# Performance work log

Hardware: AMD Instinct MI355X
Metric: run time of the kernel (lower is better)

## Reference

```python
import jax, jax.numpy as jnp
import numpy as np

MODES = (16, 16)
EMBED_DIM = 64
NUM_HEADS = 8


def spectral_conv(x, w):
    """FNO-style spectral conv. x: [B,S,Ci,H,W]; w: [Ci,Co,mx,my,2] (real/imag)."""
    wc = w[..., 0] + 1j * w[..., 1]
    H, W = x.shape[-2], x.shape[-1]
    mx, my = wc.shape[2], wc.shape[3]
    xf = jnp.fft.rfft2(x)                                   # [B,S,Ci,H,W//2+1]
    of = jnp.einsum('bsixy,ioxy->bsoxy', xf[..., :mx, :my], wc)
    out_f = jnp.zeros(x.shape[:2] + (wc.shape[1], H, W // 2 + 1), dtype=of.dtype)
    out_f = out_f.at[..., :mx, :my].set(of)
    return jnp.fft.irfft2(out_f, s=(H, W))


def log_cpb_bias(n_sub_x, n_sub_y, w1, b1, w2):
    """Swin-v2-style log-spaced continuous position bias -> [heads, S, S]."""
    cx = jnp.arange(n_sub_x, dtype=jnp.float32)
    cy = jnp.arange(n_sub_y, dtype=jnp.float32)
    coords = jnp.stack(jnp.meshgrid(cx, cy, indexing='ij'), axis=-1).reshape(-1, 2)
    rel = coords[:, None, :] - coords[None, :, :]           # [S,S,2]
    rel = jnp.sign(rel) * jnp.log1p(jnp.abs(rel))
    h = jax.nn.relu(rel @ w1 + b1)                          # [S,S,hidden]
    bias = h @ w2                                           # [S,S,heads]
    return jnp.transpose(bias, (2, 0, 1))


def _unflatten(f, num_heads, embed_dim):
    # [B,S,h*d,H,W] -> [B,h,S,d,H,W]
    B, S = f.shape[0], f.shape[1]
    f = f.reshape(B, S, num_heads, embed_dim, f.shape[-2], f.shape[-1])
    return jnp.transpose(f, (0, 2, 1, 3, 4, 5))


def setup_inputs() -> dict:
    key = jax.random.key(0)
    ks = jax.random.split(key, 9)
    B, S, D, H, W = 2, 64, EMBED_DIM, 32, 32
    hd = NUM_HEADS * D
    mx, my = MODES
    scale = 0.02
    return {
        'seq': jax.random.normal(ks[0], (B, S, D, H, W), dtype=jnp.float32),
        'wq': scale * jax.random.normal(ks[1], (D, hd, mx, my, 2), dtype=jnp.float32),
        'wk': scale * jax.random.normal(ks[2], (D, hd, mx, my, 2), dtype=jnp.float32),
        'wv': scale * jax.random.normal(ks[3], (D, hd, mx, my, 2), dtype=jnp.float32),
        'wo': scale * jax.random.normal(ks[4], (hd, D, mx, my, 2), dtype=jnp.float32),
        'cpb_w1': scale * jax.random.normal(ks[5], (2, D), dtype=jnp.float32),
        'cpb_b1': jnp.zeros((D,), dtype=jnp.float32),
        'cpb_w2': scale * jax.random.normal(ks[6], (D, NUM_HEADS), dtype=jnp.float32),
        'n_sub_x': 8,
        'n_sub_y': 8,
    }


def reference(seq, wq, wk, wv, wo, cpb_w1, cpb_b1, cpb_w2, n_sub_x, n_sub_y):
    q = _unflatten(spectral_conv(seq, wq), NUM_HEADS, EMBED_DIM)  # [B,h,S,d,H,W]
    k = _unflatten(spectral_conv(seq, wk), NUM_HEADS, EMBED_DIM)
    v = _unflatten(spectral_conv(seq, wv), NUM_HEADS, EMBED_DIM)

    bias = log_cpb_bias(n_sub_x, n_sub_y, cpb_w1, cpb_b1, cpb_w2)  # [h,S,S]

    d, H, W = q.shape[-3], q.shape[-2], q.shape[-1]
    scale = 1.0 / jnp.sqrt(jnp.asarray(d * H * W, dtype=q.dtype))
    scores = jnp.einsum('bhqdxy,bhkdxy->bhqk', q, k) * scale + bias[None]
    attn = jax.nn.softmax(scores, axis=-1)
    sa = jnp.einsum('bhqk,bhkdxy->bhqdxy', attn, v)          # [B,h,S,d,H,W]

    # _flatten: [B,h,S,d,H,W] -> [B,S,h*d,H,W]
    sa = jnp.transpose(sa, (0, 2, 1, 3, 4, 5))
    B, S = sa.shape[0], sa.shape[1]
    sa = sa.reshape(B, S, NUM_HEADS * EMBED_DIM, H, W)
    return spectral_conv(sa, wo)
```

## Files before the change

kernel.cpp:

```cpp
#include <hip/hip_runtime.h>

#define TWO_PI 6.28318530717958647692f

#define NH 8
#define CH 128
#define NCH 2

#define OFF_XM   0ull
#define OFF_WTA  (OFF_XM + 8388608ull)
#define OFF_WTB  (OFF_WTA + 16777216ull)
#define OFF_PO   (OFF_WTB + 16777216ull)
#define OFF_ATTN (OFF_PO + 16777216ull)
#define WS_TOTAL (OFF_ATTN + 262144ull)

typedef short bf16x8 __attribute__((ext_vector_type(8)));
typedef float f32x4 __attribute__((ext_vector_type(4)));
#define MFMA_B16(a, b, c) __builtin_amdgcn_mfma_f32_16x16x32_bf16(a, b, c, 0, 0, 0)

__device__ __forceinline__ float bl(unsigned u) { return __uint_as_float(u << 16); }
__device__ __forceinline__ unsigned short f2b(float f) {
    unsigned u = __float_as_uint(f);
    return (unsigned short)((u + 0x7fffu + ((u >> 16) & 1u)) >> 16);
}
__device__ __forceinline__ unsigned pack2(float lo, float hi) {
    return (unsigned)f2b(lo) | ((unsigned)f2b(hi) << 16);
}

__device__ __forceinline__ bf16x8 mkfrag(const unsigned* __restrict__ Wt, int co_l, int ri,
                                         int ci0, bool dc) {
    unsigned a0 = Wt[(ci0 + 0) * 64 + (co_l ^ (ci0 + 0))];
    unsigned a1 = Wt[(ci0 + 1) * 64 + (co_l ^ (ci0 + 1))];
    unsigned a2 = Wt[(ci0 + 2) * 64 + (co_l ^ (ci0 + 2))];
    unsigned a3 = Wt[(ci0 + 3) * 64 + (co_l ^ (ci0 + 3))];
    uint4 r;
    if (ri) {
        if (dc) { r.x = 0u; r.y = 0u; r.z = 0u; r.w = 0u; }
        else {
            r.x = (a0 >> 16) | (a0 << 16); r.y = (a1 >> 16) | (a1 << 16);
            r.z = (a2 >> 16) | (a2 << 16); r.w = (a3 >> 16) | (a3 << 16);
        }
    } else {
        r.x = a0 ^ 0x80000000u; r.y = a1 ^ 0x80000000u;
        r.z = a2 ^ 0x80000000u; r.w = a3 ^ 0x80000000u;
    }
    return __builtin_bit_cast(bf16x8, r);
}

__global__ __launch_bounds__(256) void k_transpose2(const float* __restrict__ srcA, unsigned* __restrict__ dstA, int kindA,
                                                    const float* __restrict__ srcB, unsigned* __restrict__ dstB, int kindB,
                                                    int m0) {
    const float* in = (blockIdx.z == 0) ? srcA : srcB;
    unsigned* outp = (blockIdx.z == 0) ? dstA : dstB;
    int kind = (blockIdx.z == 0) ? kindA : kindB;
    __shared__ unsigned T[16][65];
    int tid = threadIdx.x;
    int r0 = blockIdx.x * 64;
    int ci, h;
    if (kind == 2) { h = r0 >> 12; ci = (r0 >> 6) & 63; }
    else           { ci = r0 >> 9; h = (r0 >> 6) & 7; }
    int ml0 = blockIdx.y * 16;
    int u = (m0 + ml0) >> 4;
    const float4* in4 = (const float4*)in;
    float fac1 = (kind == 0) ? 1.41421356f : 1.f;
    float facu = (kind == 0) ? (u > 0 ? 0.70710678f : 1.f)
               : (kind == 1) ? (u > 0 ? 0.5f : 1.f) : 1.f;
    #pragma unroll
    for (int p = 0; p < 2; ++p) {
        int f = tid + p * 256;
        int row = f >> 3, mc2 = (f & 7) * 2;
        float4 v = in4[(size_t)(r0 + row) * 128 + ((m0 + ml0) >> 1) + (f & 7)];
        float fac0 = (mc2 > 0) ? fac1 : facu;
        T[mc2][row] = pack2(v.x * fac0, v.y * fac0);
        T[mc2 + 1][row] = pack2(v.z * fac1, v.w * fac1);
    }
    __syncthreads();
    #pragma unroll
    for (int p = 0; p < 4; ++p) {
        int f = tid + p * 256;
        int ml = f >> 6, co = f & 63;
        outp[((size_t)((ml0 + ml) * 8 + h) << 12) + ci * 64 + co] = T[ml][co];
    }
}

__global__ __launch_bounds__(256) void k_rfft_y(const float* __restrict__ seq,
                                                float2* __restrict__ T) {
    __shared__ float c32[32], s32[32];
    __shared__ float fld[32][33];
    int tid = threadIdx.x;
    int bc = blockIdx.x;
    if (tid < 32) { float s, c; __sincosf(TWO_PI * tid / 32.0f, &s, &c); c32[tid] = c; s32[tid] = s; }
    float4 v = ((const float4*)(seq + (size_t)bc * 1024))[tid];
    int x = tid >> 3, y4 = (tid & 7) * 4;
    fld[x][y4] = v.x; fld[x][y4 + 1] = v.y; fld[x][y4 + 2] = v.z; fld[x][y4 + 3] = v.w;
    __syncthreads();
    float2* op = T + (size_t)bc * 512;
    #pragma unroll
    for (int p = 0; p < 2; ++p) {
        int e = tid + p * 256;
        int xx = e >> 4, vv = e & 15;
        float sr = 0.f, si = 0.f;
        #pragma unroll
        for (int y = 0; y < 32; ++y) {
            float f = fld[xx][y];
            int ph = (vv * y) & 31;
            sr = fmaf(f, c32[ph], sr);
            si = fmaf(-f, s32[ph], si);
        }
        float2 t; t.x = sr; t.y = si;
        op[e] = t;
    }
}

__global__ __launch_bounds__(256) void k_rfft_x(const float2* __restrict__ T,
                                                unsigned short* __restrict__ XM) {
    __shared__ float c32[32], s32[32];
    __shared__ float2 t[8][512];
    int tid = threadIdx.x;
    int cig = blockIdx.x;
    int bs = blockIdx.y;
    if (tid < 32) { float s, c; __sincosf(TWO_PI * tid / 32.0f, &s, &c); c32[tid] = c; s32[tid] = s; }
    const float4* src = (const float4*)(T + ((size_t)bs * 64 + cig * 8) * 512);
    #pragma unroll
    for (int p = 0; p < 8; ++p) {
        int idx = tid + p * 256;
        float4 w = src[idx];
        int ch = idx >> 8, r2 = idx & 255;
        float2 t0; t0.x = w.x; t0.y = w.y;
        float2 t1; t1.x = w.z; t1.y = w.w;
        t[ch][r2 * 2] = t0; t[ch][r2 * 2 + 1] = t1;
    }
    __syncthreads();
    int u = tid >> 4, vv = tid & 15;
    unsigned outw[8];
    for (int ch = 0; ch < 8; ++ch) {
        float xr = 0.f, xi = 0.f;
        #pragma unroll
        for (int x = 0; x < 32; ++x) {
            float2 tv = t[ch][x * 16 + vv];
            int ph = (u * x) & 31;
            float c = c32[ph], s = s32[ph];
            xr += tv.x * c + tv.y * s;
            xi += tv.y * c - tv.x * s;
        }
        outw[ch] = pack2(xr, xi);
    }
    uint4* op = (uint4*)(XM + (((size_t)tid * 128 + bs) * 64 + cig * 8) * 2);
    uint4 a, b;
    a.x = outw[0]; a.y = outw[1]; a.z = outw[2]; a.w = outw[3];
    b.x = outw[4]; b.y = outw[5]; b.z = outw[6]; b.w = outw[7];
    op[0] = a; op[1] = b;
}

__global__ __launch_bounds__(512) void k_qks(const unsigned short* __restrict__ XM,
                                             const unsigned* __restrict__ WQ,
                                             const unsigned* __restrict__ WK,
                                             float* __restrict__ part, int mbase) {
    __shared__ __align__(16) unsigned char Xs[16384];
    __shared__ __align__(16) unsigned Wq[4096];
    __shared__ __align__(16) unsigned Wk[4096];
    unsigned char* Qs = Xs;
    unsigned char* Ks = (unsigned char*)Wq;
    int tid = threadIdx.x;
    int mg = blockIdx.x, h = blockIdx.y, b = blockIdx.z;
    int lane = tid & 63, w = tid >> 6;
    int lr = lane & 15, lg = lane >> 4;
    int wr = w & 1, wc = w >> 1;
    int sxa = (lr & 7) << 4;
    int ri = lr & 1;
    f32x4 zf = {0.f, 0.f, 0.f, 0.f};
    f32x4 sacc[2];
    sacc[0] = zf; sacc[1] = zf;
    for (int mm = 0; mm < 4; ++mm) {
        int ml = mg * 4 + mm;
        int mode = mbase + ml;
        bool dc = (mode == 0);
        __syncthreads();
        {
            const unsigned short* xg = XM + ((size_t)mode * 128 + b * 64) * 128;
            #pragma unroll
            for (int p = 0; p < 2; ++p) {
                int g = tid + p * 512; int row = g >> 4, c16 = g & 15;
                uint4 v = *(const uint4*)(xg + row * 128 + c16 * 8);
                *(uint4*)(Xs + row * 256 + ((c16 * 16) ^ ((row & 7) << 4))) = v;
            }
        }
        {
            const unsigned* tq = WQ + ((size_t)(ml * 8 + h) << 12);
            const unsigned* tk = WK + ((size_t)(ml * 8 + h) << 12);
            #pragma unroll
            for (int p = 0; p < 16; ++p) {
                int idx = tid + p * 512;
                int r = idx & 4095;
                int ci = r >> 6, co = r & 63;
                if (idx < 4096) Wq[ci * 64 + (co ^ ci)] = tq[r];
                else            Wk[ci * 64 + (co ^ ci)] = tk[r];
            }
        }
        __syncthreads();
        f32x4 qa[2][2], ka[2][2];
        {
            #pragma unroll
            for (int m = 0; m < 2; ++m)
                #pragma unroll
                for (int n = 0; n < 2; ++n) { qa[m][n] = zf; ka[m][n] = zf; }
            #pragma unroll
            for (int ks = 0; ks < 4; ++ks) {
                int kb = (ks * 64 + lg * 16) ^ sxa;
                int ci0 = ks * 16 + lg * 4;
                bf16x8 a0 = *(const bf16x8*)(Xs + (wr * 32 + lr) * 256 + kb);
                bf16x8 a1 = *(const bf16x8*)(Xs + (wr * 32 + 16 + lr) * 256 + kb);
                #pragma unroll
                for (int n = 0; n < 2; ++n) {
                    int co_l = wc * 16 + n * 8 + (lr >> 1);
                    bf16x8 bq = mkfrag(Wq, co_l, ri, ci0, dc);
                    bf16x8 bk = mkfrag(Wk, co_l, ri, ci0, dc);
                    qa[0][n] = MFMA_B16(a0, bq, qa[0][n]);
                    qa[1][n] = MFMA_B16(a1, bq, qa[1][n]);
                    ka[0][n] = MFMA_B16(a0, bk, ka[0][n]);
                    ka[1][n] = MFMA_B16(a1, bk, ka[1][n]);
                }
            }
        }
        __syncthreads();
        {
            #pragma unroll
            for (int m = 0; m < 2; ++m)
                #pragma unroll
                for (int n = 0; n < 2; ++n) {
                    int colb = (wc * 32 + n * 16 + lr) * 2;
                    #pragma unroll
                    for (int r = 0; r < 4; ++r) {
                        int row = wr * 32 + m * 16 + lg * 4 + r;
                        int swz = (row & 7) << 4;
                        *(unsigned short*)(Qs + row * 256 + (colb ^ swz)) = f2b(qa[m][n][r]);
                        *(unsigned short*)(Ks + row * 256 + (colb ^ swz)) = f2b(ka[m][n][r]);
                    }
                }
        }
        __syncthreads();
        {
            #pragma unroll
            for (int ks = 0; ks < 4; ++ks) {
                int kb = (ks * 64 + lg * 16) ^ sxa;
                bf16x8 a0 = *(const bf16x8*)(Qs + (wr * 32 + lr) * 256 + kb);
                bf16x8 a1 = *(const bf16x8*)(Qs + (wr * 32 + 16 + lr) * 256 + kb);
                bf16x8 b0 = *(const bf16x8*)(Ks + (wc * 16 + lr) * 256 + kb);
                sacc[0] = MFMA_B16(a0, b0, sacc[0]);
                sacc[1] = MFMA_B16(a1, b0, sacc[1]);
            }
        }
    }
    float* pp = part + (((size_t)((mbase >> 2) + mg) * 16 + b * 8 + h) << 12);
    #pragma unroll
    for (int m = 0; m < 2; ++m)
        #pragma unroll
        for (int r = 0; r < 4; ++r)
            pp[(wr * 32 + m * 16 + lg * 4 + r) * 64 + wc * 16 + lr] = sacc[m][r];
}

__global__ void k_softmax(const float* __restrict__ part,
                          const float* __restrict__ w1, const float* __restrict__ b1,
                          const float* __restrict__ w2, unsigned short* __restrict__ attnb) {
    int j = threadIdx.x;
    int i = blockIdx.x;
    int bh = blockIdx.y;
    int h = bh & 7;
    float s = 0.f;
    for (int mg = 0; mg < 64; ++mg)
        s += part[(((size_t)mg * 16 + bh) * 64 + i) * 64 + j];
    float dx = (float)((i >> 3) - (j >> 3));
    float dy = (float)((i & 7) - (j & 7));
    float rx = (dx > 0.f ? 1.f : (dx < 0.f ? -1.f : 0.f)) * log1pf(fabsf(dx));
    float ry = (dy > 0.f ? 1.f : (dy < 0.f ? -1.f : 0.f)) * log1pf(fabsf(dy));
    float bias = 0.f;
    for (int l = 0; l < 64; ++l) {
        float hv = fmaxf(rx * w1[l] + ry * w1[64 + l] + b1[l], 0.f);
        bias = fmaf(hv, w2[l * NH + h], bias);
    }
    s = s * (1.0f / 262144.0f) + bias;
    float m = s;
    for (int o = 32; o >= 1; o >>= 1) m = fmaxf(m, __shfl_xor(m, o));
    float e = expf(s - m);
    float t = e;
    for (int o = 32; o >= 1; o >>= 1) t += __shfl_xor(t, o);
    attnb[((size_t)bh * 64 + i) * 64 + j] = f2b(e / t);
}

__global__ __launch_bounds__(512) void k_savo(const unsigned short* __restrict__ XM,
                                              const unsigned* __restrict__ WV,
                                              const unsigned* __restrict__ WO,
                                              const unsigned short* __restrict__ attnb,
                                              float* __restrict__ outf, int mbase) {
    __shared__ __align__(16) unsigned char Xs[16384];
    __shared__ __align__(16) unsigned Wv[4096];
    __shared__ __align__(16) unsigned Wo[4096];
    unsigned char* Vt = (unsigned char*)Wv;
    unsigned char* Ss = (unsigned char*)Wv;
    int tid = threadIdx.x;
    int ml = blockIdx.x, b = blockIdx.y;
    int mode = mbase + ml;
    bool dc = (mode == 0);
    int lane = tid & 63, w = tid >> 6;
    int lr = lane & 15, lg = lane >> 4;
    int wr = w & 1, wc = w >> 1;
    int sxa = (lr & 7) << 4;
    int ri = lr & 1;
    f32x4 zf = {0.f, 0.f, 0.f, 0.f};
    {
        const unsigned short* xg = XM + ((size_t)mode * 128 + b * 64) * 128;
        #pragma unroll
        for (int p = 0; p < 2; ++p) {
            int g = tid + p * 512; int row = g >> 4, c16 = g & 15;
            uint4 v = *(const uint4*)(xg + row * 128 + c16 * 8);
            *(uint4*)(Xs + row * 256 + ((c16 * 16) ^ ((row & 7) << 4))) = v;
        }
    }
    f32x4 oacc[2][2];
    oacc[0][0] = zf; oacc[0][1] = zf; oacc[1][0] = zf; oacc[1][1] = zf;
    for (int h = 0; h < NH; ++h) {
        __syncthreads();
        {
            const unsigned* tv = WV + ((size_t)(ml * 8 + h) << 12);
            const unsigned* to = WO + ((size_t)(ml * 8 + h) << 12);
            #pragma unroll
            for (int p = 0; p < 16; ++p) {
                int idx = tid + p * 512;
                int r = idx & 4095;
                int ci = r >> 6, co = r & 63;
                if (idx < 4096) Wv[ci * 64 + (co ^ ci)] = tv[r];
                else            Wo[ci * 64 + (co ^ ci)] = to[r];
            }
        }
        bf16x8 af[2][2];
        #pragma unroll
        for (int m = 0; m < 2; ++m)
            #pragma unroll
            for (int ks = 0; ks < 2; ++ks) {
                int irow = wr * 32 + m * 16 + lr;
                af[m][ks] = *(const bf16x8*)(attnb + (((size_t)(b * 8 + h) * 64 + irow) * 64 + ks * 32 + lg * 8));
            }
        __syncthreads();
        f32x4 va[2][2];
        {
            va[0][0] = zf; va[0][1] = zf; va[1][0] = zf; va[1][1] = zf;
            #pragma unroll
            for (int ks = 0; ks < 4; ++ks) {
                int kb = (ks * 64 + lg * 16) ^ sxa;
                int ci0 = ks * 16 + lg * 4;
                bf16x8 a0 = *(const bf16x8*)(Xs + (wr * 32 + lr) * 256 + kb);
                bf16x8 a1 = *(const bf16x8*)(Xs + (wr * 32 + 16 + lr) * 256 + kb);
                #pragma unroll
                for (int n = 0; n < 2; ++n) {
                    int co_l = wc * 16 + n * 8 + (lr >> 1);
                    bf16x8 bb = mkfrag(Wv, co_l, ri, ci0, dc);
                    va[0][n] = MFMA_B16(a0, bb, va[0][n]);
                    va[1][n] = MFMA_B16(a1, bb, va[1][n]);
                }
            }
        }
        __syncthreads();
        {
            #pragma unroll
            for (int m = 0; m < 2; ++m)
                #pragma unroll
                for (int n = 0; n < 2; ++n) {
                    int cp = wc * 32 + n * 16 + lr;
                    int j0 = wr * 32 + m * 16 + lg * 4;
                    uint2 t;
                    t.x = pack2(va[m][n][0], va[m][n][1]);
                    t.y = pack2(va[m][n][2], va[m][n][3]);
                    *(uint2*)(Vt + cp * 128 + ((j0 * 2) ^ ((cp & 7) << 4))) = t;
                }
        }
        __syncthreads();
        f32x4 sa_[2][2];
        {
            sa_[0][0] = zf; sa_[0][1] = zf; sa_[1][0] = zf; sa_[1][1] = zf;
            #pragma unroll
            for (int ks = 0; ks < 2; ++ks) {
                #pragma unroll
                for (int n = 0; n < 2; ++n) {
                    int cp = wc * 32 + n * 16 + lr;
                    bf16x8 bb = *(const bf16x8*)(Vt + cp * 128 + ((ks * 64 + lg * 16) ^ ((cp & 7) << 4)));
                    sa_[0][n] = MFMA_B16(af[0][ks], bb, sa_[0][n]);
                    sa_[1][n] = MFMA_B16(af[1][ks], bb, sa_[1][n]);
                }
            }
        }
        __syncthreads();
        {
            #pragma unroll
            for (int m = 0; m < 2; ++m)
                #pragma unroll
                for (int n = 0; n < 2; ++n) {
                    int colb = (wc * 32 + n * 16 + lr) * 2;
                    #pragma unroll
                    for (int r = 0; r < 4; ++r) {
                        int row = wr * 32 + m * 16 + lg * 4 + r;
                        *(unsigned short*)(Ss + row * 256 + (colb ^ ((row & 7) << 4))) = f2b(sa_[m][n][r]);
                    }
                }
        }
        __syncthreads();
        {
            #pragma unroll
            for (int ks = 0; ks < 4; ++ks) {
                int kb = (ks * 64 + lg * 16) ^ sxa;
                int ci0 = ks * 16 + lg * 4;
                bf16x8 a0 = *(const bf16x8*)(Ss + (wr * 32 + lr) * 256 + kb);
                bf16x8 a1 = *(const bf16x8*)(Ss + (wr * 32 + 16 + lr) * 256 + kb);
                #pragma unroll
                for (int n = 0; n < 2; ++n) {
                    int co_l = wc * 16 + n * 8 + (lr >> 1);
                    bf16x8 bb = mkfrag(Wo, co_l, ri, ci0, false);
                    oacc[0][n] = MFMA_B16(a0, bb, oacc[0][n]);
                    oacc[1][n] = MFMA_B16(a1, bb, oacc[1][n]);
                }
            }
        }
    }
    #pragma unroll
    for (int m = 0; m < 2; ++m)
        #pragma unroll
        for (int n = 0; n < 2; ++n)
            #pragma unroll
            for (int r = 0; r < 4; ++r) {
                int i = wr * 32 + m * 16 + lg * 4 + r;
                int c2p = wc * 32 + n * 16 + lr;
                outf[((size_t)mode * 128 + b * 64 + i) * 128 + c2p] = oacc[m][n][r];
            }
}

__global__ __launch_bounds__(256) void k_irfft_v(const float* __restrict__ outf,
                                                 float2* __restrict__ G) {
    __shared__ float c32[32], s32[32];
    __shared__ float2 mf[256][8];
    int tid = threadIdx.x;
    int cg = blockIdx.x;
    int bs = blockIdx.y;
    if (tid < 32) { float s, c; __sincosf(TWO_PI * tid / 32.0f, &s, &c); c32[tid] = c; s32[tid] = s; }
    #pragma unroll
    for (int p = 0; p < 4; ++p) {
        int idx = tid + p * 256;
        int mode = idx >> 2, q = idx & 3;
        float4 v = *(const float4*)(outf + ((size_t)mode * 128 + bs) * 128 + cg * 16 + q * 4);
        float2 t0; t0.x = v.x; t0.y = v.y;
        float2 t1; t1.x = v.z; t1.y = v.w;
        mf[mode][q * 2] = t0; mf[mode][q * 2 + 1] = t1;
    }
    __syncthreads();
    #pragma unroll 1
    for (int p = 0; p < 2; ++p) {
        int e = tid + p * 256;
        int u = e >> 5, y = e & 31;
        #pragma unroll 1
        for (int ch = 0; ch < 8; ++ch) {
            float2 f0 = mf[u * 16][ch];
            float fr0 = f0.x;
            float fi0 = (u == 0) ? 0.f : f0.y;
            float ssr = 0.5f * fr0, ssi = 0.5f * fi0;
            #pragma unroll
            for (int v = 1; v < 16; ++v) {
                float2 f = mf[u * 16 + v][ch];
                int ph = (v * y) & 31;
                float c = c32[ph], s = s32[ph];
                ssr += f.x * c - f.y * s;
                ssi += f.x * s + f.y * c;
            }
            float2 g; g.x = ssr; g.y = ssi;
            G[(((size_t)u * 128 + bs) * 64 + cg * 8 + ch) * 32 + y] = g;
        }
    }
}

__global__ __launch_bounds__(256) void k_irfft_u(const float2* __restrict__ G,
                                                 float* __restrict__ out) {
    __shared__ float c32[32], s32[32];
    __shared__ float2 Gs[16][8][32];
    int tid = threadIdx.x;
    int cg = blockIdx.x;
    int bs = blockIdx.y;
    if (tid < 32) { float s, c; __sincosf(TWO_PI * tid / 32.0f, &s, &c); c32[tid] = c; s32[tid] = s; }
    #pragma unroll
    for (int p = 0; p < 8; ++p) {
        int idx = tid + p * 256;
        int y2 = idx & 15, ch = (idx >> 4) & 7, u = idx >> 7;
        float4 v = *(const float4*)((const float*)G + ((((size_t)u * 128 + bs) * 64 + cg * 8 + ch) * 32 + y2 * 2) * 2);
        float2 t0; t0.x = v.x; t0.y = v.y;
        float2 t1; t1.x = v.z; t1.y = v.w;
        Gs[u][ch][y2 * 2] = t0; Gs[u][ch][y2 * 2 + 1] = t1;
    }
    __syncthreads();
    #pragma unroll 1
    for (int p = 0; p < 4; ++p) {
        int pos = tid + p * 256;
        int x = pos >> 5, y = pos & 31;
        #pragma unroll 1
        for (int ch = 0; ch < 8; ++ch) {
            float acc = 0.f;
            #pragma unroll
            for (int u = 0; u < 16; ++u) {
                float2 g = Gs[u][ch][y];
                int ph = (u * x) & 31;
                acc += g.x * c32[ph] - g.y * s32[ph];
            }
            out[((size_t)(bs * 64 + cg * 8 + ch)) * 1024 + x * 32 + y] = acc * (1.0f / 512.0f);
        }
    }
}

extern "C" void kernel_launch(void* const* d_in, const int* in_sizes, int n_in,
                              void* d_out, int out_size, void* d_ws, size_t ws_size,
                              hipStream_t stream) {
    (void)in_sizes; (void)n_in; (void)out_size;
    const float* seq = (const float*)d_in[0];
    const float* wq = (const float*)d_in[1];
    const float* wk = (const float*)d_in[2];
    const float* wv = (const float*)d_in[3];
    const float* wo = (const float*)d_in[4];
    const float* cw1 = (const float*)d_in[5];
    const float* cb1 = (const float*)d_in[6];
    const float* cw2 = (const float*)d_in[7];
    float* out = (float*)d_out;
    char* ws = (char*)d_ws;
    if (ws_size < WS_TOTAL) return;

    unsigned short* XM = (unsigned short*)(ws + OFF_XM);
    unsigned* WTA = (unsigned*)(ws + OFF_WTA);
    unsigned* WTB = (unsigned*)(ws + OFF_WTB);
    float2* Tbuf = (float2*)(ws + OFF_WTA);
    float2* G = (float2*)(ws + OFF_WTA);
    float* PART = (float*)(ws + OFF_PO);
    float* OUTF = (float*)(ws + OFF_PO);
    unsigned short* ATTNB = (unsigned short*)(ws + OFF_ATTN);

    k_rfft_y<<<dim3(8192), dim3(256), 0, stream>>>(seq, Tbuf);
    k_rfft_x<<<dim3(8, 128), dim3(256), 0, stream>>>(Tbuf, XM);

    for (int c = 0; c < NCH; ++c) {
        int m0 = c * CH;
        k_transpose2<<<dim3(512, CH / 16, 2), dim3(256), 0, stream>>>(wq, WTA, 0, wk, WTB, 0, m0);
        k_qks<<<dim3(CH / 4, NH, 2), dim3(512), 0, stream>>>(XM, WTA, WTB, PART, m0);
    }
    k_softmax<<<dim3(64, 16), dim3(64), 0, stream>>>(PART, cw1, cb1, cw2, ATTNB);

    for (int c = 0; c < NCH; ++c) {
        int m0 = c * CH;
        k_transpose2<<<dim3(512, CH / 16, 2), dim3(256), 0, stream>>>(wv, WTA, 1, wo, WTB, 2, m0);
        k_savo<<<dim3(CH, 2), dim3(512), 0, stream>>>(XM, WTA, WTB, ATTNB, OUTF, m0);
    }
    k_irfft_v<<<dim3(8, 128), dim3(256), 0, stream>>>(OUTF, G);
    k_irfft_u<<<dim3(8, 128), dim3(256), 0, stream>>>(G, out);
}
```

Before: 335.8 us.

## Pre-swizzle spectral layouts in global memory and stage tiles via direct global-to-LDS loads

The producer kernels now write the weight tables and the mode-major spectral activations in the XOR-swizzled order that the shared-memory tiles expect. The consumer kernels can then copy tiles with 16-byte direct global-to-LDS loads instead of a register round trip with per-element swizzled stores. This removes VGPR staging and scalar 4-byte weight stores in the hot loops of the QK and output kernels. It depends on the global_load_lds intrinsic with 16-byte width and on the pre-swizzled layouts matching the read-side indexing exactly.

```diff
diff --git a/kernel.cpp b/kernel.cpp
--- a/kernel.cpp
+++ b/kernel.cpp
@@ -16,6 +16,10 @@
 typedef short bf16x8 __attribute__((ext_vector_type(8)));
 typedef float f32x4 __attribute__((ext_vector_type(4)));
 #define MFMA_B16(a, b, c) __builtin_amdgcn_mfma_f32_16x16x32_bf16(a, b, c, 0, 0, 0)
+
+#define G2L(g, l) __builtin_amdgcn_global_load_lds( \
+    (const __attribute__((address_space(1))) void*)(g), \
+    (__attribute__((address_space(3))) void*)(l), 16, 0, 0)
 
 __device__ __forceinline__ float bl(unsigned u) { return __uint_as_float(u << 16); }
 __device__ __forceinline__ unsigned short f2b(float f) {
@@ -78,7 +82,7 @@
     for (int p = 0; p < 4; ++p) {
         int f = tid + p * 256;
         int ml = f >> 6, co = f & 63;
-        outp[((size_t)((ml0 + ml) * 8 + h) << 12) + ci * 64 + co] = T[ml][co];
+        outp[((size_t)((ml0 + ml) * 8 + h) << 12) + ci * 64 + (co ^ ci)] = T[ml][co];
     }
 }
 
@@ -144,11 +148,13 @@
         }
         outw[ch] = pack2(xr, xi);
     }
-    uint4* op = (uint4*)(XM + (((size_t)tid * 128 + bs) * 64 + cig * 8) * 2);
+    unsigned short* rowp = XM + ((size_t)tid * 128 + bs) * 128;
     uint4 a, b;
     a.x = outw[0]; a.y = outw[1]; a.z = outw[2]; a.w = outw[3];
     b.x = outw[4]; b.y = outw[5]; b.z = outw[6]; b.w = outw[7];
-    op[0] = a; op[1] = b;
+    int sw = bs & 7;
+    *(uint4*)(rowp + ((cig * 2) ^ sw) * 8) = a;
+    *(uint4*)(rowp + ((cig * 2 + 1) ^ sw) * 8) = b;
 }
 
 __global__ __launch_bounds__(512) void k_qks(const unsigned short* __restrict__ XM,
@@ -176,24 +182,15 @@
         bool dc = (mode == 0);
         __syncthreads();
         {
-            const unsigned short* xg = XM + ((size_t)mode * 128 + b * 64) * 128;
+            const char* xg = (const char*)(XM + ((size_t)mode * 128 + b * 64) * 128);
+            const char* tq = (const char*)(WQ + ((size_t)(ml * 8 + h) << 12));
+            const char* tk = (const char*)(WK + ((size_t)(ml * 8 + h) << 12));
             #pragma unroll
             for (int p = 0; p < 2; ++p) {
-                int g = tid + p * 512; int row = g >> 4, c16 = g & 15;
-                uint4 v = *(const uint4*)(xg + row * 128 + c16 * 8);
-                *(uint4*)(Xs + row * 256 + ((c16 * 16) ^ ((row & 7) << 4))) = v;
-            }
-        }
-        {
-            const unsigned* tq = WQ + ((size_t)(ml * 8 + h) << 12);
-            const unsigned* tk = WK + ((size_t)(ml * 8 + h) << 12);
-            #pragma unroll
-            for (int p = 0; p < 16; ++p) {
-                int idx = tid + p * 512;
-                int r = idx & 4095;
-                int ci = r >> 6, co = r & 63;
-                if (idx < 4096) Wq[ci * 64 + (co ^ ci)] = tq[r];
-                else            Wk[ci * 64 + (co ^ ci)] = tk[r];
+                int off = (tid + p * 512) * 16;
+                G2L(xg + off, Xs + off);
+                G2L(tq + off, (char*)Wq + off);
+                G2L(tk + off, (char*)Wk + off);
             }
         }
         __syncthreads();
@@ -307,12 +304,11 @@
     int ri = lr & 1;
     f32x4 zf = {0.f, 0.f, 0.f, 0.f};
     {
-        const unsigned short* xg = XM + ((size_t)mode * 128 + b * 64) * 128;
+        const char* xg = (const char*)(XM + ((size_t)mode * 128 + b * 64) * 128);
         #pragma unroll
         for (int p = 0; p < 2; ++p) {
-            int g = tid + p * 512; int row = g >> 4, c16 = g & 15;
-            uint4 v = *(const uint4*)(xg + row * 128 + c16 * 8);
-            *(uint4*)(Xs + row * 256 + ((c16 * 16) ^ ((row & 7) << 4))) = v;
+            int off = (tid + p * 512) * 16;
+            G2L(xg + off, Xs + off);
         }
     }
     f32x4 oacc[2][2];
@@ -320,15 +316,13 @@
     for (int h = 0; h < NH; ++h) {
         __syncthreads();
         {
-            const unsigned* tv = WV + ((size_t)(ml * 8 + h) << 12);
-            const unsigned* to = WO + ((size_t)(ml * 8 + h) << 12);
-            #pragma unroll
-            for (int p = 0; p < 16; ++p) {
-                int idx = tid + p * 512;
-                int r = idx & 4095;
-                int ci = r >> 6, co = r & 63;
-                if (idx < 4096) Wv[ci * 64 + (co ^ ci)] = tv[r];
-                else            Wo[ci * 64 + (co ^ ci)] = to[r];
+            const char* tv = (const char*)(WV + ((size_t)(ml * 8 + h) << 12));
+            const char* to = (const char*)(WO + ((size_t)(ml * 8 + h) << 12));
+            #pragma unroll
+            for (int p = 0; p < 2; ++p) {
+                int off = (tid + p * 512) * 16;
+                G2L(tv + off, (char*)Wv + off);
+                G2L(to + off, (char*)Wo + off);
             }
         }
         bf16x8 af[2][2];
```

Result: faster. 321.1 us, median of 3 (-4.4%).
